# Kernel tuning notes

Measured on AMD Instinct MI355X. Metric: run time of the kernel, lower is better.

## Reference

```python
import jax, jax.numpy as jnp
import numpy as np

G, N, E = 16, 512, 2048        # graphs, nodes/graph, edges/graph
CN, CE = 64, 64                # node / edge feature channels
K = 3                          # Laguerre polynomial order
RATIO = 0.5
KEEP = int(np.ceil(RATIO * N)) # 256 kept nodes per graph (static)
POWER_ITERS = 64               # power iteration approximating eigsh(k=1,'LM')


def setup_inputs() -> dict:
    key = jax.random.key(0)
    ks = jax.random.split(key, 10)
    x_n = jax.random.normal(ks[0], (G * N, CN), jnp.float32)
    x_e = jax.random.normal(ks[1], (G * E, CE), jnp.float32)
    # incidence endpoints per edge, local node ids, no self loops
    u = jax.random.randint(ks[2], (G, E), 0, N)
    v = (u + 1 + jax.random.randint(ks[3], (G, E), 0, N - 1)) % N
    # node-level conv graph (global ids within per-graph blocks): both directions
    offs = (jnp.arange(G) * N)[:, None]
    src_n = jnp.concatenate([(u + offs).reshape(-1), (v + offs).reshape(-1)])
    dst_n = jnp.concatenate([(v + offs).reshape(-1), (u + offs).reshape(-1)])
    edge_weight_n = jax.random.uniform(ks[4], (src_n.shape[0],), jnp.float32)
    # edge-level conv graph (global ids within per-graph edge blocks)
    ME = 4 * E
    offs_e = (jnp.arange(G) * E)[:, None]
    src_e = (jax.random.randint(ks[5], (G, ME), 0, E) + offs_e).reshape(-1)
    dst_e = (jax.random.randint(ks[6], (G, ME), 0, E) + offs_e).reshape(-1)
    edge_weight_e = jax.random.uniform(ks[7], (src_e.shape[0],), jnp.float32)
    # HodgeLaguerreConv(C -> 1, K) weights (glorot-ish) + bias (zeros init)
    W_n = jax.random.normal(ks[8], (K, CN), jnp.float32) / np.sqrt(CN)
    b_n = jnp.zeros((1,), jnp.float32)
    W_e = jax.random.normal(ks[9], (K, CE), jnp.float32) / np.sqrt(CE)
    b_e = jnp.zeros((1,), jnp.float32)
    return dict(x_n=x_n, x_e=x_e, edge_u=u, edge_v=v,
                src_n=src_n, dst_n=dst_n, edge_weight_n=edge_weight_n,
                src_e=src_e, dst_e=dst_e, edge_weight_e=edge_weight_e,
                W_n=W_n, b_n=b_n, W_e=W_e, b_e=b_e)


def hodge_laguerre(x, src, dst, w, Wk, b):
    """HodgeLaguerreConv with out_channels=1: out = sum_k T_k(L) x @ Wk[k] + b.
    T_0 = x; T_1 = x - Lx; T_{k+1} = (-L T_k + (2k+1) T_k - k T_{k-1})/(k+1)."""
    num = x.shape[0]
    def L(z):  # scatter-add message passing: out[i] = sum_{j->i} norm * z[j]
        return jax.ops.segment_sum(w[:, None] * z[src], dst, num_segments=num)
    Tx0 = x
    out = Tx0 @ Wk[0]
    Tx1 = x - L(x)
    out = out + Tx1 @ Wk[1]
    k = 1
    for i in range(2, Wk.shape[0]):
        Tx2 = (-L(Tx1) + (2 * k + 1) * Tx1 - k * Tx0) / (k + 1)
        out = out + Tx2 @ Wk[i]
        Tx0, Tx1 = Tx1, Tx2
        k += 1
    return out + b[0]


def pool_graph(sn, se, xn, xe, u, v):
    # node score augmented by |B1| @ edge_score (abs incidence gathers both endpoints)
    aug = sn.at[u].add(se).at[v].add(se)
    perm = jnp.argsort(-aug)                    # descending sort, take top KEEP
    mask_n = jnp.zeros((N,), xn.dtype).at[perm[:KEEP]].set(1.0)
    # mask_e = |B1|^T (1 - mask_n); keep edge iff both endpoints kept (== 0)
    bad = (1.0 - mask_n[u]) + (1.0 - mask_n[v])
    keep_e = (bad == 0.0).astype(xn.dtype)
    # dense incidence B1 [N, E]: -1 at source row, +1 at target row
    cols = jnp.arange(E)
    B = jnp.zeros((N, E), xn.dtype).at[u, cols].add(-1.0).at[v, cols].add(1.0)
    Bm = B * mask_n[:, None] * keep_e[None, :]  # row/col masking (zero-padded)
    L0 = Bm @ Bm.T                              # [N, N] node Laplacian
    L1 = Bm.T @ Bm                              # [E, E] edge Laplacian
    # power iteration for lambda_max(L0) (== eigsh k=1 'LM'; zero rows keep spectrum)
    w = jnp.ones((N,), xn.dtype) / np.sqrt(N)
    for _ in range(POWER_ITERS):
        w = L0 @ w
        w = w / (jnp.linalg.norm(w) + 1e-12)
    lam = w @ (L0 @ w)
    scale = 2.0 / (lam + 1e-12)
    return xn * mask_n[:, None], L0 * scale, xe * keep_e[:, None], L1 * scale


def reference(x_n, x_e, edge_u, edge_v, src_n, dst_n, edge_weight_n,
              src_e, dst_e, edge_weight_e, W_n, b_n, W_e, b_e):
    score_n = jax.nn.sigmoid(hodge_laguerre(x_n, src_n, dst_n, edge_weight_n, W_n, b_n).reshape(-1))
    score_e = jax.nn.sigmoid(hodge_laguerre(x_e, src_e, dst_e, edge_weight_e, W_e, b_e).reshape(-1))
    xn_g = (x_n * score_n[:, None]).reshape(G, N, CN)
    xe_g = (x_e * score_e[:, None]).reshape(G, E, CE)
    sn = score_n.reshape(G, N)
    se = score_e.reshape(G, E)
    return jax.vmap(pool_graph)(sn, se, xn_g, xe_g, edge_u, edge_v)
```

## Files before the change

### kernel.cpp

```cpp
#include <hip/hip_runtime.h>
#include <math.h>

#define GG 16
#define NNODE 512
#define EEDGE 2048
#define KEEPN 256
#define PITERS 64
#define NNT 8192
#define NET 32768

typedef float vfloat4 __attribute__((ext_vector_type(4)));

#define WS_C1N 0
#define WS_C2N 8192
#define WS_BN  16384
#define WS_C1E 24576
#define WS_C2E 57344
#define WS_BE  90112
#define WS_SNW 122880
#define WS_SEW 131072
#define WS_KLIST 163840
#define WS_KCNT 196608
#define WS_SCALE 196624

#define O_XN 0
#define O_L0 524288
#define O_XE 4718592
#define O_L1 6815744

#define L04 1048576
#define ZTOT4 17825792

#define DCAP 12

__global__ __launch_bounds__(512) void k_dots(
    const float* __restrict__ xn, const float* __restrict__ xe,
    const float* __restrict__ Wn, const float* __restrict__ We,
    float* __restrict__ ws) {
  const int tid = threadIdx.x, bid = blockIdx.x;
  const int lane = tid & 63;
  const int wv = (bid * 512 + tid) >> 6;
  #pragma unroll
  for (int n = 0; n < 5; ++n) {
    int gw = wv + n * 8192;
    const float* x; const float* W; int row; float *c1, *c2, *bs;
    if (gw < NNT) {
      row = gw; x = xn + (size_t)row * 64; W = Wn;
      c1 = ws + WS_C1N; c2 = ws + WS_C2N; bs = ws + WS_BN;
    } else {
      row = gw - NNT;
      x = xe + (size_t)row * 64; W = We;
      c1 = ws + WS_C1E; c2 = ws + WS_C2E; bs = ws + WS_BE;
    }
    float v = x[lane];
    float r0 = v * W[lane];
    float r1 = v * W[64 + lane];
    float r2 = v * W[128 + lane];
    for (int o = 32; o; o >>= 1) {
      r0 += __shfl_xor(r0, o, 64);
      r1 += __shfl_xor(r1, o, 64);
      r2 += __shfl_xor(r2, o, 64);
    }
    if (lane == 0) { c1[row] = r1; c2[row] = r2; bs[row] = r0 + r1 + r2; }
  }
}

#define SM_AUG 0
#define SM_SNW 512
#define SM_RED 1024
#define SM_IWS 1032
#define SM_KCP 1040
#define SM_S0  1056
#define SM_TOT 9256
__global__ __launch_bounds__(512, 2) void k_pipe(
    const int* __restrict__ src_n, const int* __restrict__ dst_n, const float* __restrict__ wn,
    const int* __restrict__ src_e, const int* __restrict__ dst_e, const float* __restrict__ we,
    const int* __restrict__ edge_u, const int* __restrict__ edge_v,
    const float* __restrict__ bnp, const float* __restrict__ bep,
    float* __restrict__ ws, float* __restrict__ out) {
  const int tid = threadIdx.x;
  if (blockIdx.x >= 16) {
    vfloat4 z = (vfloat4)(0.f);
    vfloat4* o4 = (vfloat4*)out;
    int base = (blockIdx.x - 16) * 512 + tid;
    #pragma unroll
    for (int n = 0; n < 17; ++n) {
      int i = base + n * 1048576;
      int f = (i < L04) ? (O_L0 / 4 + i) : (O_L1 / 4 + (i - L04));
      __builtin_nontemporal_store(z, &o4[f]);
    }
    return;
  }
  __shared__ float smem[SM_TOT];
  int* smi = (int*)smem;
  float* aug = smem + SM_AUG;
  float* snw = smem + SM_SNW;
  float* red = smem + SM_RED;
  int*   iws = smi + SM_IWS;
  int*   kcp = smi + SM_KCP;

  const int g = blockIdx.x;
  const int roffN = g * NNODE;
  const int roffE = g * EEDGE;
  const int lane = tid & 63, wid = tid >> 6;
  float biasN = bnp[0], biasE = bep[0];

  {
    float* c1n = smem + SM_S0;
    float* c2n = smem + SM_S0 + 512;
    float* d1n = smem + SM_S0 + 1024;
    float* d2n = smem + SM_S0 + 1536;
    float* e2n = smem + SM_S0 + 2048;
    c1n[tid] = ws[WS_C1N + roffN + tid];
    c2n[tid] = ws[WS_C2N + roffN + tid];
    d1n[tid] = 0.f; d2n[tid] = 0.f; e2n[tid] = 0.f;
    int sN[8], dN[8]; float wN[8];
    #pragma unroll
    for (int n = 0; n < 8; ++n) {
      int t = tid + n * 512;
      int idx = (n < 4) ? (g * 2048 + t) : (32768 + g * 2048 + (t - 2048));
      sN[n] = src_n[idx] - roffN; dN[n] = dst_n[idx] - roffN; wN[n] = wn[idx];
    }
    __syncthreads();
    #pragma unroll
    for (int n = 0; n < 8; ++n) {
      atomicAdd(&d1n[dN[n]], wN[n] * c1n[sN[n]]);
      atomicAdd(&d2n[dN[n]], wN[n] * c2n[sN[n]]);
    }
    __syncthreads();
    #pragma unroll
    for (int n = 0; n < 8; ++n)
      atomicAdd(&e2n[dN[n]], wN[n] * d2n[sN[n]]);
    __syncthreads();
    float t = ws[WS_BN + roffN + tid] - d1n[tid] - 2.0f * d2n[tid]
            + 0.5f * e2n[tid] + biasN;
    float s = 1.0f / (1.0f + expf(-t));
    snw[tid] = s; aug[tid] = s;
    __syncthreads();
  }

  float* seS = smem + SM_S0 + 2048;
  int*   suv = smi + SM_S0;
  {
    float* c1e = smem + SM_S0;
    float* c2e = smem + SM_S0 + 2048;
    float* d1e = smem + SM_S0 + 4096;
    float* d2e = smem + SM_S0 + 6144;
    float* e2e = smem + SM_S0;
    {
      float4 a = ((const float4*)(ws + WS_C1E + roffE))[tid];
      float4 b = ((const float4*)(ws + WS_C2E + roffE))[tid];
      ((float4*)c1e)[tid] = a;
      ((float4*)c2e)[tid] = b;
      ((float4*)d1e)[tid] = make_float4(0.f, 0.f, 0.f, 0.f);
      ((float4*)d2e)[tid] = make_float4(0.f, 0.f, 0.f, 0.f);
    }
    int sE[16], dE[16]; float wE[16];
    #pragma unroll
    for (int n = 0; n < 16; ++n) {
      int idx = g * 8192 + n * 512 + tid;
      sE[n] = src_e[idx] - roffE; dE[n] = dst_e[idx] - roffE; wE[n] = we[idx];
    }
    __syncthreads();
    #pragma unroll
    for (int n = 0; n < 16; ++n) {
      atomicAdd(&d1e[dE[n]], wE[n] * c1e[sE[n]]);
      atomicAdd(&d2e[dE[n]], wE[n] * c2e[sE[n]]);
    }
    __syncthreads();
    ((float4*)e2e)[tid] = make_float4(0.f, 0.f, 0.f, 0.f);
    __syncthreads();
    #pragma unroll
    for (int n = 0; n < 16; ++n)
      atomicAdd(&e2e[dE[n]], wE[n] * d2e[sE[n]]);
    float bR[4]; int uR[4], vR[4];
    #pragma unroll
    for (int n = 0; n < 4; ++n) {
      int e = tid + n * 512;
      bR[n] = ws[WS_BE + roffE + e];
      uR[n] = edge_u[roffE + e];
      vR[n] = edge_v[roffE + e];
    }
    __syncthreads();
    #pragma unroll
    for (int n = 0; n < 4; ++n) {
      int e = tid + n * 512;
      float t = bR[n] - d1e[e] - 2.0f * d2e[e] + 0.5f * e2e[e] + biasE;
      float s = 1.0f / (1.0f + expf(-t));
      seS[e] = s;
      suv[e] = uR[n] | (vR[n] << 16);
      atomicAdd(&aug[uR[n]], s);
      atomicAdd(&aug[vR[n]], s);
    }
    __syncthreads();
  }

  unsigned short* adjU = (unsigned short*)(smem + SM_S0 + 4096);
  float* wvA = smem + SM_S0 + 6144;
  float* wvB = smem + SM_S0 + 6660;
  int* maskS = smi + SM_S0 + 7176;
  int* degS  = smi + SM_S0 + 7688;
  int* offS  = smi + SM_SNW;

  {
    float a = aug[tid];
    int r = 0;
    #pragma unroll 8
    for (int j = 0; j < NNODE; ++j) {
      float b = aug[j];
      r += (b > a) || (b == a && j < tid);
    }
    maskS[tid] = (r < KEEPN) ? 1 : 0;
    degS[tid] = 0;
  }
  if (tid == 0) *kcp = 0;
  __syncthreads();
  ws[WS_SNW + roffN + tid] = snw[tid] * (float)maskS[tid];

  int* wsi = (int*)ws;
  for (int e = tid; e < EEDGE; e += 512) {
    int p2 = suv[e];
    int u = p2 & 0xffff, v = p2 >> 16;
    int k = maskS[u] & maskS[v];
    ws[WS_SEW + roffE + e] = seS[e] * (float)k;
    if (k) {
      int p = atomicAdd(kcp, 1);
      wsi[WS_KLIST + roffE + p] = e;
      atomicAdd(&degS[u], 1);
      atomicAdd(&degS[v], 1);
    }
  }
  __syncthreads();
  if (tid == 0) wsi[WS_KCNT + g] = *kcp;

  int dv = degS[tid];
  int inc = dv;
  for (int o = 1; o < 64; o <<= 1) {
    int t = __shfl_up(inc, o, 64);
    if (lane >= o) inc += t;
  }
  if (lane == 63) iws[wid] = inc;
  __syncthreads();
  int base = 0;
  for (int k = 0; k < wid; ++k) base += iws[k];
  int myStart = base + inc - dv;
  offS[tid] = myStart;
  __syncthreads();

  for (int e = tid; e < EEDGE; e += 512) {
    int p2 = suv[e];
    int u = p2 & 0xffff, v = p2 >> 16;
    if (maskS[u] & maskS[v]) {
      int pu = atomicAdd(&offS[u], 1); adjU[pu] = (unsigned short)v;
      int pv = atomicAdd(&offS[v], 1); adjU[pv] = (unsigned short)u;
    }
  }
  __syncthreads();
  int myDeg = dv;
  int myEnd = myStart + myDeg;

  int nbr[DCAP];
  #pragma unroll
  for (int k = 0; k < DCAP; ++k)
    nbr[k] = (k < myDeg) ? (int)adjU[myStart + k] : NNODE;
  bool ovf = myDeg > DCAP;

  wvA[tid] = 0.04419417382415922f;
  if (tid == 0) { wvA[NNODE] = 0.f; wvB[NNODE] = 0.f; }
  __syncthreads();
  float* wcur = wvA; float* wnext = wvB;
  for (int it = 0; it < PITERS; ++it) {
    float tg[DCAP];
    #pragma unroll
    for (int k = 0; k < DCAP; ++k) tg[k] = wcur[nbr[k]];
    float acc = (float)myDeg * wcur[tid];
    #pragma unroll
    for (int k = 0; k < DCAP; ++k) acc -= tg[k];
    if (ovf) for (int p = myStart + DCAP; p < myEnd; ++p) acc -= wcur[(int)adjU[p]];
    if ((it & 7) == 7) {
      float sq = acc * acc;
      for (int o = 32; o; o >>= 1) sq += __shfl_xor(sq, o, 64);
      if (lane == 0) red[wid] = sq;
      __syncthreads();
      float tot = red[0] + red[1] + red[2] + red[3]
                + red[4] + red[5] + red[6] + red[7];
      wnext[tid] = acc * (1.0f / (sqrtf(tot) + 1e-12f));
    } else {
      wnext[tid] = acc;
    }
    __syncthreads();
    float* tmp = wcur; wcur = wnext; wnext = tmp;
  }
  {
    float tg[DCAP];
    #pragma unroll
    for (int k = 0; k < DCAP; ++k) tg[k] = wcur[nbr[k]];
    float wv_ = wcur[tid];
    float acc = (float)myDeg * wv_;
    #pragma unroll
    for (int k = 0; k < DCAP; ++k) acc -= tg[k];
    if (ovf) for (int p = myStart + DCAP; p < myEnd; ++p) acc -= wcur[(int)adjU[p]];
    float pr = wv_ * acc;
    for (int o = 32; o; o >>= 1) pr += __shfl_xor(pr, o, 64);
    if (lane == 0) red[wid] = pr;
    __syncthreads();
    if (tid == 0) {
      float lam = red[0] + red[1] + red[2] + red[3]
                + red[4] + red[5] + red[6] + red[7];
      ws[WS_SCALE + g] = 2.0f / (lam + 1e-12f);
    }
  }
}

__global__ __launch_bounds__(256) void k_out(
    const float* __restrict__ xn, const float* __restrict__ xe,
    const int* __restrict__ edge_u, const int* __restrict__ edge_v,
    const float* __restrict__ ws, float* __restrict__ out) {
  int b = blockIdx.x, tid = threadIdx.x;
  const int* wsi = (const int*)ws;
  if (b < 512) {
    int idx = b * 256 + tid;
    int row = idx >> 4;
    float s = ws[WS_SNW + row];
    float4 x4 = ((const float4*)xn)[idx];
    ((float4*)(out + O_XN))[idx] = make_float4(x4.x * s, x4.y * s, x4.z * s, x4.w * s);
  } else if (b < 2560) {
    int idx = (b - 512) * 256 + tid;
    int row = idx >> 4;
    float s = ws[WS_SEW + row];
    float4 x4 = ((const float4*)xe)[idx];
    ((float4*)(out + O_XE))[idx] = make_float4(x4.x * s, x4.y * s, x4.z * s, x4.w * s);
  } else if (b < 2576) {
    int g = b - 2560;
    int cnt = wsi[WS_KCNT + g];
    float s = ws[WS_SCALE + g];
    float* L0 = out + O_L0 + (long long)g * (NNODE * NNODE);
    const int* kl = wsi + WS_KLIST + g * EEDGE;
    const int* eu = edge_u + g * EEDGE;
    const int* ev = edge_v + g * EEDGE;
    for (int t = tid; t < cnt; t += 256) {
      int e = kl[t];
      int u = eu[e], v = ev[e];
      atomicAdd(&L0[u * NNODE + u], s);
      atomicAdd(&L0[v * NNODE + v], s);
      atomicAdd(&L0[u * NNODE + v], -s);
      atomicAdd(&L0[v * NNODE + u], -s);
    }
  } else {
    int q = b - 2576;
    int g = q >> 8, sb = q & 255;
    int cnt = wsi[WS_KCNT + g];
    float s = ws[WS_SCALE + g];
    float* L1 = out + O_L1 + (long long)g * (EEDGE * EEDGE);
    const int* kl = wsi + WS_KLIST + g * EEDGE;
    const int* eu = edge_u + g * EEDGE;
    const int* ev = edge_v + g * EEDGE;
    for (int a = sb; a < cnt; a += 256) {
      int e1 = kl[a];
      int u1 = eu[e1], v1 = ev[e1];
      long long rowoff = (long long)e1 * EEDGE;
      for (int b2 = tid; b2 < cnt; b2 += 256) {
        int e2 = kl[b2];
        int u2 = eu[e2], v2 = ev[e2];
        int val = (u1 == u2) + (v1 == v2) - (v1 == u2) - (u1 == v2);
        if (val) L1[rowoff + e2] = s * (float)val;
      }
    }
  }
}

extern "C" void kernel_launch(void* const* d_in, const int* in_sizes, int n_in,
                              void* d_out, int out_size, void* d_ws, size_t ws_size,
                              hipStream_t stream) {
  const float* x_n = (const float*)d_in[0];
  const float* x_e = (const float*)d_in[1];
  const int* edge_u = (const int*)d_in[2];
  const int* edge_v = (const int*)d_in[3];
  const int* src_n = (const int*)d_in[4];
  const int* dst_n = (const int*)d_in[5];
  const float* ew_n = (const float*)d_in[6];
  const int* src_e = (const int*)d_in[7];
  const int* dst_e = (const int*)d_in[8];
  const float* ew_e = (const float*)d_in[9];
  const float* W_n = (const float*)d_in[10];
  const float* b_n = (const float*)d_in[11];
  const float* W_e = (const float*)d_in[12];
  const float* b_e = (const float*)d_in[13];
  float* ws = (float*)d_ws;
  float* out = (float*)d_out;

  k_dots<<<1024, 512, 0, stream>>>(x_n, x_e, W_n, W_e, ws);
  k_pipe<<<16 + 2048, 512, 0, stream>>>(src_n, dst_n, ew_n, src_e, dst_e, ew_e,
                                        edge_u, edge_v, b_n, b_e, ws, out);
  k_out<<<6672, 256, 0, stream>>>(x_n, x_e, edge_u, edge_v, ws, out);
}
```

Measured before the change: 455.2 us.

## Split per-graph message passing into grid-wide atomic kernels before pooling

Moves the Laguerre message-passing and scoring out of the 16-block per-graph pipeline kernel into three grid-wide kernels (two scatter passes with global atomics and a score kernel). Accumulators live in scratch space carved from the L0 output region, which k_dots zeroes first and k_pool later overwrites. The aim is to spread the serial per-graph scatter work across many more blocks instead of 16. The cost is three extra launches and contended global atomics in place of shared-memory atomics.

```diff
diff --git a/kernel.cpp b/kernel.cpp
--- a/kernel.cpp
+++ b/kernel.cpp
@@ -28,6 +28,14 @@
 #define O_XE 4718592
 #define O_L1 6815744
 
+#define AC_D1N 0
+#define AC_D2N 8192
+#define AC_E2N 16384
+#define AC_D1E 24576
+#define AC_D2E 57344
+#define AC_E2E 90112
+#define AC_TOT4 30720
+
 #define L04 1048576
 #define ZTOT4 17825792
 
@@ -36,8 +44,16 @@
 __global__ __launch_bounds__(512) void k_dots(
     const float* __restrict__ xn, const float* __restrict__ xe,
     const float* __restrict__ Wn, const float* __restrict__ We,
-    float* __restrict__ ws) {
+    float* __restrict__ ws, float* __restrict__ out) {
   const int tid = threadIdx.x, bid = blockIdx.x;
+  if (bid >= 1024) {
+    vfloat4 z = (vfloat4)(0.f);
+    vfloat4* a4 = (vfloat4*)(out + O_L0);
+    int base = (bid - 1024) * 512 + tid;
+    #pragma unroll
+    for (int k = 0; k < 4; ++k) a4[base + k * 7680] = z;
+    return;
+  }
   const int lane = tid & 63;
   const int wv = (bid * 512 + tid) >> 6;
   #pragma unroll
@@ -65,18 +81,81 @@
   }
 }
 
-#define SM_AUG 0
-#define SM_SNW 512
-#define SM_RED 1024
-#define SM_IWS 1032
-#define SM_KCP 1040
-#define SM_S0  1056
-#define SM_TOT 9256
-__global__ __launch_bounds__(512, 2) void k_pipe(
+__global__ __launch_bounds__(512) void k_mp1(
     const int* __restrict__ src_n, const int* __restrict__ dst_n, const float* __restrict__ wn,
     const int* __restrict__ src_e, const int* __restrict__ dst_e, const float* __restrict__ we,
+    const float* __restrict__ ws, float* __restrict__ out) {
+  int gid = blockIdx.x * 512 + threadIdx.x;
+  float* acc = (float*)(out + O_L0);
+  if (gid < 65536) {
+    int s = src_n[gid], d = dst_n[gid]; float w = wn[gid];
+    atomicAdd(&acc[AC_D1N + d], w * ws[WS_C1N + s]);
+    atomicAdd(&acc[AC_D2N + d], w * ws[WS_C2N + s]);
+  } else {
+    int e = gid - 65536;
+    int s = src_e[e], d = dst_e[e]; float w = we[e];
+    atomicAdd(&acc[AC_D1E + d], w * ws[WS_C1E + s]);
+    atomicAdd(&acc[AC_D2E + d], w * ws[WS_C2E + s]);
+  }
+}
+
+__global__ __launch_bounds__(512) void k_mp2(
+    const int* __restrict__ src_n, const int* __restrict__ dst_n, const float* __restrict__ wn,
+    const int* __restrict__ src_e, const int* __restrict__ dst_e, const float* __restrict__ we,
+    float* __restrict__ ws, float* __restrict__ out) {
+  int gid = blockIdx.x * 512 + threadIdx.x;
+  float* acc = (float*)(out + O_L0);
+  if (gid < 8192) ws[WS_C1N + gid] = 0.f;
+  if (gid < 65536) {
+    int s = src_n[gid], d = dst_n[gid]; float w = wn[gid];
+    atomicAdd(&acc[AC_E2N + d], w * acc[AC_D2N + s]);
+  } else {
+    int e = gid - 65536;
+    int s = src_e[e], d = dst_e[e]; float w = we[e];
+    atomicAdd(&acc[AC_E2E + d], w * acc[AC_D2E + s]);
+  }
+}
+
+__global__ __launch_bounds__(512) void k_score(
     const int* __restrict__ edge_u, const int* __restrict__ edge_v,
     const float* __restrict__ bnp, const float* __restrict__ bep,
+    float* __restrict__ ws, float* __restrict__ out) {
+  int gid = blockIdx.x * 512 + threadIdx.x;
+  const float* acc = (const float*)(out + O_L0);
+  if (gid < 8192) {
+    int i = gid;
+    float t = ws[WS_BN + i] - acc[AC_D1N + i] - 2.0f * acc[AC_D2N + i]
+            + 0.5f * acc[AC_E2N + i] + bnp[0];
+    float s = 1.0f / (1.0f + expf(-t));
+    ws[WS_SNW + i] = s;
+    atomicAdd(&ws[WS_C1N + i], s);
+  } else {
+    int e = gid - 8192;
+    float t = ws[WS_BE + e] - acc[AC_D1E + e] - 2.0f * acc[AC_D2E + e]
+            + 0.5f * acc[AC_E2E + e] + bep[0];
+    float s = 1.0f / (1.0f + expf(-t));
+    ws[WS_SEW + e] = s;
+    int g = e >> 11;
+    int u = edge_u[e], v = edge_v[e];
+    atomicAdd(&ws[WS_C1N + g * NNODE + u], s);
+    atomicAdd(&ws[WS_C1N + g * NNODE + v], s);
+  }
+}
+
+#define PM_AUG  0
+#define PM_RED  512
+#define PM_IWS  520
+#define PM_KCP  528
+#define PM_MASK 544
+#define PM_DEG  1056
+#define PM_OFF  1568
+#define PM_SUV  2080
+#define PM_ADJ  4128
+#define PM_WVA  6176
+#define PM_WVB  6692
+#define PM_TOT  7208
+__global__ __launch_bounds__(512, 2) void k_pool(
+    const int* __restrict__ edge_u, const int* __restrict__ edge_v,
     float* __restrict__ ws, float* __restrict__ out) {
   const int tid = threadIdx.x;
   if (blockIdx.x >= 16) {
@@ -91,116 +170,30 @@
     }
     return;
   }
-  __shared__ float smem[SM_TOT];
+  __shared__ float smem[PM_TOT];
   int* smi = (int*)smem;
-  float* aug = smem + SM_AUG;
-  float* snw = smem + SM_SNW;
-  float* red = smem + SM_RED;
-  int*   iws = smi + SM_IWS;
-  int*   kcp = smi + SM_KCP;
+  float* aug = smem + PM_AUG;
+  float* red = smem + PM_RED;
+  int* iws   = smi + PM_IWS;
+  int* kcp   = smi + PM_KCP;
+  int* maskS = smi + PM_MASK;
+  int* degS  = smi + PM_DEG;
+  int* offS  = smi + PM_OFF;
+  int* suv   = smi + PM_SUV;
+  unsigned short* adjU = (unsigned short*)(smi + PM_ADJ);
+  float* wvA = smem + PM_WVA;
+  float* wvB = smem + PM_WVB;
 
   const int g = blockIdx.x;
   const int roffN = g * NNODE;
   const int roffE = g * EEDGE;
   const int lane = tid & 63, wid = tid >> 6;
-  float biasN = bnp[0], biasE = bep[0];
-
-  {
-    float* c1n = smem + SM_S0;
-    float* c2n = smem + SM_S0 + 512;
-    float* d1n = smem + SM_S0 + 1024;
-    float* d2n = smem + SM_S0 + 1536;
-    float* e2n = smem + SM_S0 + 2048;
-    c1n[tid] = ws[WS_C1N + roffN + tid];
-    c2n[tid] = ws[WS_C2N + roffN + tid];
-    d1n[tid] = 0.f; d2n[tid] = 0.f; e2n[tid] = 0.f;
-    int sN[8], dN[8]; float wN[8];
-    #pragma unroll
-    for (int n = 0; n < 8; ++n) {
-      int t = tid + n * 512;
-      int idx = (n < 4) ? (g * 2048 + t) : (32768 + g * 2048 + (t - 2048));
-      sN[n] = src_n[idx] - roffN; dN[n] = dst_n[idx] - roffN; wN[n] = wn[idx];
-    }
-    __syncthreads();
-    #pragma unroll
-    for (int n = 0; n < 8; ++n) {
-      atomicAdd(&d1n[dN[n]], wN[n] * c1n[sN[n]]);
-      atomicAdd(&d2n[dN[n]], wN[n] * c2n[sN[n]]);
-    }
-    __syncthreads();
-    #pragma unroll
-    for (int n = 0; n < 8; ++n)
-      atomicAdd(&e2n[dN[n]], wN[n] * d2n[sN[n]]);
-    __syncthreads();
-    float t = ws[WS_BN + roffN + tid] - d1n[tid] - 2.0f * d2n[tid]
-            + 0.5f * e2n[tid] + biasN;
-    float s = 1.0f / (1.0f + expf(-t));
-    snw[tid] = s; aug[tid] = s;
-    __syncthreads();
-  }
-
-  float* seS = smem + SM_S0 + 2048;
-  int*   suv = smi + SM_S0;
-  {
-    float* c1e = smem + SM_S0;
-    float* c2e = smem + SM_S0 + 2048;
-    float* d1e = smem + SM_S0 + 4096;
-    float* d2e = smem + SM_S0 + 6144;
-    float* e2e = smem + SM_S0;
-    {
-      float4 a = ((const float4*)(ws + WS_C1E + roffE))[tid];
-      float4 b = ((const float4*)(ws + WS_C2E + roffE))[tid];
-      ((float4*)c1e)[tid] = a;
-      ((float4*)c2e)[tid] = b;
-      ((float4*)d1e)[tid] = make_float4(0.f, 0.f, 0.f, 0.f);
-      ((float4*)d2e)[tid] = make_float4(0.f, 0.f, 0.f, 0.f);
-    }
-    int sE[16], dE[16]; float wE[16];
-    #pragma unroll
-    for (int n = 0; n < 16; ++n) {
-      int idx = g * 8192 + n * 512 + tid;
-      sE[n] = src_e[idx] - roffE; dE[n] = dst_e[idx] - roffE; wE[n] = we[idx];
-    }
-    __syncthreads();
-    #pragma unroll
-    for (int n = 0; n < 16; ++n) {
-      atomicAdd(&d1e[dE[n]], wE[n] * c1e[sE[n]]);
-      atomicAdd(&d2e[dE[n]], wE[n] * c2e[sE[n]]);
-    }
-    __syncthreads();
-    ((float4*)e2e)[tid] = make_float4(0.f, 0.f, 0.f, 0.f);
-    __syncthreads();
-    #pragma unroll
-    for (int n = 0; n < 16; ++n)
-      atomicAdd(&e2e[dE[n]], wE[n] * d2e[sE[n]]);
-    float bR[4]; int uR[4], vR[4];
-    #pragma unroll
-    for (int n = 0; n < 4; ++n) {
-      int e = tid + n * 512;
-      bR[n] = ws[WS_BE + roffE + e];
-      uR[n] = edge_u[roffE + e];
-      vR[n] = edge_v[roffE + e];
-    }
-    __syncthreads();
-    #pragma unroll
-    for (int n = 0; n < 4; ++n) {
-      int e = tid + n * 512;
-      float t = bR[n] - d1e[e] - 2.0f * d2e[e] + 0.5f * e2e[e] + biasE;
-      float s = 1.0f / (1.0f + expf(-t));
-      seS[e] = s;
-      suv[e] = uR[n] | (vR[n] << 16);
-      atomicAdd(&aug[uR[n]], s);
-      atomicAdd(&aug[vR[n]], s);
-    }
-    __syncthreads();
-  }
-
-  unsigned short* adjU = (unsigned short*)(smem + SM_S0 + 4096);
-  float* wvA = smem + SM_S0 + 6144;
-  float* wvB = smem + SM_S0 + 6660;
-  int* maskS = smi + SM_S0 + 7176;
-  int* degS  = smi + SM_S0 + 7688;
-  int* offS  = smi + SM_SNW;
+
+  float snw_r = ws[WS_SNW + roffN + tid];
+  aug[tid] = ws[WS_C1N + roffN + tid];
+  if (tid == 0) *kcp = 0;
+  degS[tid] = 0;
+  __syncthreads();
 
   {
     float a = aug[tid];
@@ -211,23 +204,33 @@
       r += (b > a) || (b == a && j < tid);
     }
     maskS[tid] = (r < KEEPN) ? 1 : 0;
-    degS[tid] = 0;
-  }
-  if (tid == 0) *kcp = 0;
-  __syncthreads();
-  ws[WS_SNW + roffN + tid] = snw[tid] * (float)maskS[tid];
+  }
+  __syncthreads();
+  ws[WS_SNW + roffN + tid] = snw_r * (float)maskS[tid];
 
   int* wsi = (int*)ws;
-  for (int e = tid; e < EEDGE; e += 512) {
-    int p2 = suv[e];
-    int u = p2 & 0xffff, v = p2 >> 16;
-    int k = maskS[u] & maskS[v];
-    ws[WS_SEW + roffE + e] = seS[e] * (float)k;
-    if (k) {
-      int p = atomicAdd(kcp, 1);
-      wsi[WS_KLIST + roffE + p] = e;
-      atomicAdd(&degS[u], 1);
-      atomicAdd(&degS[v], 1);
+  {
+    float seR[4]; int uR[4], vR[4];
+    #pragma unroll
+    for (int n = 0; n < 4; ++n) {
+      int e = tid + n * 512;
+      seR[n] = ws[WS_SEW + roffE + e];
+      uR[n] = edge_u[roffE + e];
+      vR[n] = edge_v[roffE + e];
+    }
+    #pragma unroll
+    for (int n = 0; n < 4; ++n) {
+      int e = tid + n * 512;
+      int u = uR[n], v = vR[n];
+      suv[e] = u | (v << 16);
+      int k = maskS[u] & maskS[v];
+      ws[WS_SEW + roffE + e] = seR[n] * (float)k;
+      if (k) {
+        int p = atomicAdd(kcp, 1);
+        wsi[WS_KLIST + roffE + p] = e;
+        atomicAdd(&degS[u], 1);
+        atomicAdd(&degS[v], 1);
+      }
     }
   }
   __syncthreads();
@@ -389,8 +392,10 @@
   float* ws = (float*)d_ws;
   float* out = (float*)d_out;
 
-  k_dots<<<1024, 512, 0, stream>>>(x_n, x_e, W_n, W_e, ws);
-  k_pipe<<<16 + 2048, 512, 0, stream>>>(src_n, dst_n, ew_n, src_e, dst_e, ew_e,
-                                        edge_u, edge_v, b_n, b_e, ws, out);
+  k_dots<<<1024 + 15, 512, 0, stream>>>(x_n, x_e, W_n, W_e, ws, out);
+  k_mp1<<<384, 512, 0, stream>>>(src_n, dst_n, ew_n, src_e, dst_e, ew_e, ws, out);
+  k_mp2<<<384, 512, 0, stream>>>(src_n, dst_n, ew_n, src_e, dst_e, ew_e, ws, out);
+  k_score<<<80, 512, 0, stream>>>(edge_u, edge_v, b_n, b_e, ws, out);
+  k_pool<<<16 + 2048, 512, 0, stream>>>(edge_u, edge_v, ws, out);
   k_out<<<6672, 256, 0, stream>>>(x_n, x_e, edge_u, edge_v, ws, out);
 }
```

Measured after the change: 419.1 us. 7.9% less time.
